# Performance work log

Measured on AMD Instinct MI355X. Metric: run time of the kernel, lower is better.

Reference implementation:

```python
import jax, jax.numpy as jnp
import numpy as np
import math

B, S, F, D, H, L, E, K = 8, 1024, 8, 512, 8, 3, 4, 2
HD = D // H


def _ln(x, g, b, eps=1e-5):
    m = x.mean(-1, keepdims=True)
    v = x.var(-1, keepdims=True)
    return (x - m) / jnp.sqrt(v + eps) * g + b


def _pos_encoding(seq, d):
    pos = jnp.arange(seq, dtype=jnp.float32)[:, None]
    div = jnp.exp(jnp.arange(0, d, 2, dtype=jnp.float32) * (-math.log(10000.0) / d))
    pe = jnp.zeros((seq, d), jnp.float32)
    pe = pe.at[:, 0::2].set(jnp.sin(pos * div))
    pe = pe.at[:, 1::2].set(jnp.cos(pos * div))
    return pe


def setup_inputs() -> dict:
    key = jax.random.key(0)
    ks = iter(jax.random.split(key, 40))

    def w(shape, s=0.02):
        return jax.random.normal(next(ks), shape, jnp.float32) * s

    return {
        "x": jax.random.normal(next(ks), (B, S, F), jnp.float32),
        "Wp": w((D, F)), "bp": jnp.zeros((D,), jnp.float32),
        "femb": w((5, D)),
        "qkv_w": w((L, 3 * D, D)), "qkv_b": jnp.zeros((L, 3 * D), jnp.float32),
        "ow": w((L, D, D)), "ob": jnp.zeros((L, D), jnp.float32),
        "g1": jnp.ones((L, D), jnp.float32), "beta1": jnp.zeros((L, D), jnp.float32),
        "gw": w((L, E, D)), "gb": jnp.zeros((L, E), jnp.float32),
        "ew1": w((L, E, 2 * D, D)), "eb1": jnp.zeros((L, E, 2 * D), jnp.float32),
        "ew2": w((L, E, D, 2 * D)), "eb2": jnp.zeros((L, E, D), jnp.float32),
        "g2": jnp.ones((L, D), jnp.float32), "beta2": jnp.zeros((L, D), jnp.float32),
        "hw": w((3, D)), "hb": jnp.zeros((3,), jnp.float32),
        "freq_idx": 2,
    }


def reference(x, Wp, bp, femb, qkv_w, qkv_b, ow, ob, g1, beta1, gw, gb,
              ew1, eb1, ew2, eb2, g2, beta2, hw, hb, freq_idx):
    # instance norm over time axis (torch std is unbiased -> ddof=1)
    mean = x.mean(axis=1, keepdims=True)
    std = x.std(axis=1, ddof=1, keepdims=True) + 1e-5
    xn = (x - mean) / std

    h = xn @ Wp.T + bp                      # [B,S,D]
    h = h + femb[freq_idx]                  # broadcast freq embedding
    h = h + _pos_encoding(S, D)

    for l in range(L):
        # --- multi-head self-attention ---
        qkv = h @ qkv_w[l].T + qkv_b[l]     # [B,S,3D]
        q, k, v = jnp.split(qkv, 3, axis=-1)
        q = q.reshape(B, S, H, HD).transpose(0, 2, 1, 3)
        k = k.reshape(B, S, H, HD).transpose(0, 2, 1, 3)
        v = v.reshape(B, S, H, HD).transpose(0, 2, 1, 3)
        att = jax.nn.softmax(jnp.einsum('bhqd,bhkd->bhqk', q, k) / math.sqrt(HD), axis=-1)
        o = jnp.einsum('bhqk,bhkd->bhqd', att, v).transpose(0, 2, 1, 3).reshape(B, S, D)
        o = o @ ow[l].T + ob[l]
        h = _ln(h + o, g1[l], beta1[l])

        # --- SparseMoE: top-k softmax gating, renormalized combine ---
        flat = h.reshape(-1, D)                               # [T,D], T=B*S
        probs = jax.nn.softmax(flat @ gw[l].T + gb[l], axis=-1)
        tw, ti = jax.lax.top_k(probs, K)                      # [T,K]
        tw = tw / tw.sum(axis=-1, keepdims=True)
        hid = jax.nn.relu(jnp.einsum('td,efd->tef', flat, ew1[l]) + eb1[l])  # [T,E,2D]
        eo = jnp.einsum('tef,edf->ted', hid, ew2[l]) + eb2[l]                # [T,E,D]
        cw = (jax.nn.one_hot(ti, E, dtype=flat.dtype) * tw[..., None]).sum(1)  # [T,E]
        moe = jnp.einsum('te,ted->td', cw, eo).reshape(B, S, D)
        h = _ln(h + moe, g2[l], beta2[l])

    return h[:, -1, :] @ hw.T + hb           # [B,3] quantiles
```

## Files before the change

kernel.cpp:

```cpp
#include <hip/hip_runtime.h>
#include <hip/hip_bf16.h>
#include <math.h>

typedef __hip_bfloat16 bf16;
typedef __attribute__((ext_vector_type(8))) short short8;
typedef __attribute__((ext_vector_type(4))) short s4v;
typedef __attribute__((ext_vector_type(4))) float f32x4;

constexpr int B_ = 8, S_ = 1024, F_ = 8, D_ = 512, H_ = 8, E_ = 4;
constexpr int T_  = B_ * S_;
constexpr int D3_ = 3 * D_;
constexpr int CAP_ = T_ * 2 + E_ * 128;

__device__ __forceinline__ float b2f(bf16 v) { return __bfloat162float(v); }
__device__ __forceinline__ float ldin(const void* p, size_t i, int bf) {
  return bf ? __bfloat162float(((const bf16*)p)[i]) : ((const float*)p)[i];
}
__device__ __forceinline__ void gload16(const void* g, void* l) {
  __builtin_amdgcn_global_load_lds((const __attribute__((address_space(1))) unsigned int*)g,
                                   (__attribute__((address_space(3))) unsigned int*)l, 16, 0, 0);
}

__global__ void detect_kernel(const void* __restrict__ x, int* __restrict__ flag) {
  if (threadIdx.x == 0 && blockIdx.x == 0) {
    const unsigned short* u = (const unsigned short*)x;
    int c = 0;
    for (int i = 0; i < 256; i += 2) {
      int ex = (u[i] >> 7) & 0xFF;
      if (ex >= 96 && ex <= 144) c++;
    }
    flag[0] = (c >= 64) ? 1 : 0;
  }
}

__global__ __launch_bounds__(256) void convw_kernel(const void* __restrict__ Asrc, size_t offA,
                                                    size_t nA,
                                                    const void* __restrict__ Bsrc, size_t offB,
                                                    bf16* __restrict__ dst,
                                                    const int* __restrict__ flag) {
  const int bf = flag[0];
  size_t i = ((size_t)blockIdx.x * 256 + threadIdx.x) * 8;
  const void* s = Asrc;
  size_t so = offA + i;
  if (i >= nA) { s = Bsrc; so = offB + (i - nA); }
  if (bf) {
    *(short8*)(dst + i) = *(const short8*)((const bf16*)s + so);
  } else {
    const float* sp = (const float*)s + so;
    short8 v;
#pragma unroll
    for (int u = 0; u < 8; u++) { bf16 t = __float2bfloat16(sp[u]); v[u] = *(short*)&t; }
    *(short8*)(dst + i) = v;
  }
}

__global__ __launch_bounds__(256) void instnorm_kernel(const void* __restrict__ x,
                                                       float* __restrict__ xn,
                                                       const int* __restrict__ flag) {
  const int bf = flag[0];
  int b = blockIdx.x / F_, f = blockIdx.x % F_;
  int tid = threadIdx.x;
  __shared__ float red[256];
  const int base = b * S_ * F_ + f;
  float s = 0.f;
  for (int j = tid; j < S_; j += 256) s += ldin(x, base + j * F_, bf);
  red[tid] = s; __syncthreads();
  for (int w = 128; w; w >>= 1) { if (tid < w) red[tid] += red[tid + w]; __syncthreads(); }
  float mean = red[0] / S_;
  __syncthreads();
  float v = 0.f;
  for (int j = tid; j < S_; j += 256) { float d = ldin(x, base + j * F_, bf) - mean; v += d * d; }
  red[tid] = v; __syncthreads();
  for (int w = 128; w; w >>= 1) { if (tid < w) red[tid] += red[tid + w]; __syncthreads(); }
  float inv = 1.f / (sqrtf(red[0] / (float)(S_ - 1)) + 1e-5f);
  for (int j = tid; j < S_; j += 256) xn[base + j * F_] = (ldin(x, base + j * F_, bf) - mean) * inv;
}

__global__ __launch_bounds__(256) void pe_kernel(const void* __restrict__ bp,
                                                 const void* __restrict__ femb,
                                                 const int* __restrict__ freq_idx,
                                                 float* __restrict__ addtab,
                                                 const int* __restrict__ flag) {
  const int bf = flag[0];
  int idx = blockIdx.x * 256 + threadIdx.x;
  int dp = idx & (D_ / 2 - 1);
  int s  = idx / (D_ / 2);
  int d0 = dp * 2;
  int fi = freq_idx[0];
  const float cexp = -9.2103403719761836f / (float)D_;
  float ang = (float)s * expf((float)d0 * cexp);
  float sv, cv;
  sincosf(ang, &sv, &cv);
  addtab[(size_t)s * D_ + d0]     = sv + ldin(bp, d0, bf)     + ldin(femb, (size_t)fi * D_ + d0, bf);
  addtab[(size_t)s * D_ + d0 + 1] = cv + ldin(bp, d0 + 1, bf) + ldin(femb, (size_t)fi * D_ + d0 + 1, bf);
}

constexpr int IPG_ = 8;
__global__ __launch_bounds__(256) void input_proj_kernel(const float* __restrict__ xn,
                                                         const void* __restrict__ Wp,
                                                         const float* __restrict__ addtab,
                                                         float* __restrict__ h,
                                                         bf16* __restrict__ hb16,
                                                         const int* __restrict__ flag) {
  const int bf = flag[0];
  const int tid = threadIdx.x;
  const int d0 = tid * 2;
  const int tbase = blockIdx.x * IPG_;
  float wp0[8], wp1[8];
  if (bf) {
    short8 w0 = *(const short8*)((const bf16*)Wp + (size_t)d0 * F_);
    short8 w1 = *(const short8*)((const bf16*)Wp + (size_t)(d0 + 1) * F_);
#pragma unroll
    for (int f = 0; f < 8; f++) {
      unsigned short u0 = (unsigned short)w0[f], u1 = (unsigned short)w1[f];
      wp0[f] = __bfloat162float(*(bf16*)&u0);
      wp1[f] = __bfloat162float(*(bf16*)&u1);
    }
  } else {
    const float* wpf = (const float*)Wp + (size_t)d0 * F_;
    f32x4 a = *(const f32x4*)(wpf);
    f32x4 b = *(const f32x4*)(wpf + 4);
    f32x4 c = *(const f32x4*)(wpf + 8);
    f32x4 d = *(const f32x4*)(wpf + 12);
#pragma unroll
    for (int f = 0; f < 4; f++) { wp0[f] = a[f]; wp0[4 + f] = b[f]; wp1[f] = c[f]; wp1[4 + f] = d[f]; }
  }
#pragma unroll
  for (int g = 0; g < IPG_; g++) {
    int t = tbase + g;
    int s = t & (S_ - 1);
    const float* xr = xn + (size_t)t * F_;
    f32x4 x0 = *(const f32x4*)xr;
    f32x4 x1 = *(const f32x4*)(xr + 4);
    const float2 at = *(const float2*)(addtab + (size_t)s * D_ + d0);
    float a0 = at.x, a1 = at.y;
#pragma unroll
    for (int f = 0; f < 4; f++) { a0 += x0[f] * wp0[f]; a1 += x0[f] * wp1[f]; }
#pragma unroll
    for (int f = 0; f < 4; f++) { a0 += x1[f] * wp0[4 + f]; a1 += x1[f] * wp1[4 + f]; }
    *(float2*)(h + (size_t)t * D_ + d0) = make_float2(a0, a1);
    bf16 b0 = __float2bfloat16(a0), b1 = __float2bfloat16(a1);
    unsigned pk = (unsigned)(*(unsigned short*)&b0) | ((unsigned)(*(unsigned short*)&b1) << 16);
    *(unsigned*)(hb16 + (size_t)t * D_ + d0) = pk;
  }
}

template <int MODE>
__global__ __launch_bounds__(256) void mfma_gemm(
    const bf16* __restrict__ A, const bf16* __restrict__ Wt,
    const void* __restrict__ bias, size_t boff, void* __restrict__ C_,
    int Kd, int lda, int ldb, int ldc, const int* __restrict__ flag) {
  const int wbf = flag[0];
  __shared__ bf16 As[3][128][32];
  __shared__ bf16 Bs[3][128][32];
  const int tid = threadIdx.x;
  const int ln = tid & 63, wv = tid >> 6;
  int id = blockIdx.x + gridDim.x * blockIdx.y;
  int xcd = id & 7, idq = id >> 3;
  const int n0 = (idq % gridDim.x) * 128;
  const int m0 = (xcd + 8 * (idq / gridDim.x)) * 128;
  const int wr = (wv >> 1) * 64, wc = (wv & 1) * 64;
  const int mrow = ln & 15, quad = ln >> 4;
  const int srow = ln >> 2;
  const int skof = (ln & 3) * 8;
  const int kchunk = Kd / gridDim.z;
  const int kbeg = blockIdx.z * kchunk;
  const int kend = kbeg + kchunk;

  auto stage = [&](int pb, int k0) {
#pragma unroll
    for (int j = 0; j < 2; j++) {
      int row = 16 * (4 * j + wv) + srow;
      gload16(A + (size_t)(m0 + row) * lda + k0 + skof,
              (char*)&As[pb][0][0] + (size_t)(4 * j + wv) * 1024);
    }
#pragma unroll
    for (int j = 0; j < 2; j++) {
      int row = 16 * (4 * j + wv) + srow;
      gload16(Wt + (size_t)(n0 + row) * ldb + k0 + skof,
              (char*)&Bs[pb][0][0] + (size_t)(4 * j + wv) * 1024);
    }
  };

  f32x4 acc[4][4];
#pragma unroll
  for (int i = 0; i < 4; i++)
#pragma unroll
    for (int j = 0; j < 4; j++) acc[i][j] = (f32x4){0.f, 0.f, 0.f, 0.f};

  stage(0, kbeg);
  stage(1, kbeg + 32);
  int p = 0;
  for (int k0 = kbeg; k0 < kend; k0 += 32) {
    if (k0 + 32 < kend) asm volatile("s_waitcnt vmcnt(4)" ::: "memory");
    else                asm volatile("s_waitcnt vmcnt(0)" ::: "memory");
    __builtin_amdgcn_s_barrier();
    __builtin_amdgcn_sched_barrier(0);
    short8 af[4], bfr[4];
#pragma unroll
    for (int t = 0; t < 4; t++) {
      af[t]  = *(const short8*)&As[p][wr + t * 16 + mrow][quad * 8];
      bfr[t] = *(const short8*)&Bs[p][wc + t * 16 + mrow][quad * 8];
    }
    if (k0 + 64 < kend) {
      int ps = (p == 0) ? 2 : p - 1;
      stage(ps, k0 + 64);
    }
#pragma unroll
    for (int i = 0; i < 4; i++)
#pragma unroll
      for (int j = 0; j < 4; j++)
        acc[i][j] = __builtin_amdgcn_mfma_f32_16x16x32_bf16(af[i], bfr[j], acc[i][j], 0, 0, 0);
    p = (p == 2) ? 0 : p + 1;
  }

  bf16* slice = (MODE == 0) ? (bf16*)C_ + (size_t)blockIdx.z * T_ * D_ : (bf16*)C_;
#pragma unroll
  for (int tj = 0; tj < 4; tj++) {
    int n = n0 + wc + tj * 16 + mrow;
    float bv = (MODE == 3) ? ldin(bias, boff + n, wbf) : 0.f;
#pragma unroll
    for (int ti = 0; ti < 4; ti++) {
      int mbase = m0 + wr + ti * 16 + quad * 4;
#pragma unroll
      for (int r = 0; r < 4; r++) {
        int m = mbase + r;
        float v = acc[ti][tj][r];
        slice[(size_t)m * ldc + n] = __float2bfloat16(MODE == 3 ? v + bv : v);
      }
    }
  }
}

__global__ __launch_bounds__(256) void attn_kernel(const bf16* __restrict__ qkv,
                                                   bf16* __restrict__ o) {
  __shared__ bf16 QP[64][72];
  __shared__ bf16 Ks[64][72];
  __shared__ bf16 Vt[64][72];
  const int tid = threadIdx.x;
  const int ln = tid & 63, wv = tid >> 6;
  const int mrow = ln & 15, quad = ln >> 4;
  const int id = blockIdx.x;
  const int xcd = id & 7, j = id >> 3;
  const int qt = j & 15;
  const int pr = xcd + 8 * (j >> 4);
  const int hh = pr & 7, b = pr >> 3;
  const int q0 = qt * 64;
  const int sr = tid >> 2;
  const int sg = tid & 3;
  const int sc = sg * 8;
  const int col0 = sr ^ (sg << 4);
  const int col1 = sr ^ (((sg + 4) & 3) << 4);

  {
    const bf16* src = qkv + (size_t)(b * S_ + q0 + sr) * D3_ + hh * 64;
    *(short8*)&QP[sr][sc]      = *(const short8*)(src + sc);
    *(short8*)&QP[sr][sc + 32] = *(const short8*)(src + sc + 32);
  }
  __syncthreads();
  short8 aq[2];
  aq[0] = *(const short8*)&QP[wv * 16 + mrow][quad * 8];
  aq[1] = *(const short8*)&QP[wv * 16 + mrow][quad * 8 + 32];

  float m_st = -1e30f, l_st = 0.f;
  f32x4 oacc[4];
#pragma unroll
  for (int t = 0; t < 4; t++) oacc[t] = (f32x4){0.f, 0.f, 0.f, 0.f};

  short8 kA, kB, vA, vB;
  {
    const bf16* srcK = qkv + (size_t)(b * S_ + sr) * D3_ + D_ + hh * 64;
    kA = *(const short8*)(srcK + sc);
    kB = *(const short8*)(srcK + sc + 32);
    const bf16* srcV = qkv + (size_t)(b * S_ + sr) * D3_ + 2 * D_ + hh * 64;
    vA = *(const short8*)(srcV + sc);
    vB = *(const short8*)(srcV + sc + 32);
  }

  for (int kt = 0; kt < 16; kt++) {
    __builtin_amdgcn_s_barrier();
    *(short8*)&Ks[sr][sc]      = kA;
    *(short8*)&Ks[sr][sc + 32] = kB;
#pragma unroll
    for (int u = 0; u < 8; u++) {
      *(short*)&Vt[sc + u][col0]      = vA[u];
      *(short*)&Vt[sc + 32 + u][col1] = vB[u];
    }
    if (kt + 1 < 16) {
      int k0n = (kt + 1) * 64;
      const bf16* srcK = qkv + (size_t)(b * S_ + k0n + sr) * D3_ + D_ + hh * 64;
      kA = *(const short8*)(srcK + sc);
      kB = *(const short8*)(srcK + sc + 32);
      const bf16* srcV = qkv + (size_t)(b * S_ + k0n + sr) * D3_ + 2 * D_ + hh * 64;
      vA = *(const short8*)(srcV + sc);
      vB = *(const short8*)(srcV + sc + 32);
    }
    asm volatile("s_waitcnt lgkmcnt(0)" ::: "memory");
    __builtin_amdgcn_s_barrier();
    __builtin_amdgcn_sched_barrier(0);
    f32x4 s[4];
    __builtin_amdgcn_s_setprio(1);
#pragma unroll
    for (int t = 0; t < 4; t++) {
      s[t] = (f32x4){0.f, 0.f, 0.f, 0.f};
#pragma unroll
      for (int ks = 0; ks < 2; ks++) {
        short8 bk = *(const short8*)&Ks[t * 16 + mrow][quad * 8 + ks * 32];
        s[t] = __builtin_amdgcn_mfma_f32_16x16x32_bf16(bk, aq[ks], s[t], 0, 0, 0);
      }
    }
    __builtin_amdgcn_s_setprio(0);
    float rm = s[0][0];
#pragma unroll
    for (int t = 0; t < 4; t++)
#pragma unroll
      for (int r = 0; r < 4; r++) rm = fmaxf(rm, s[t][r]);
    rm *= 0.125f;
    rm = fmaxf(rm, __shfl_xor(rm, 16, 64));
    rm = fmaxf(rm, __shfl_xor(rm, 32, 64));
    float mnew = fmaxf(m_st, rm);
    float alpha = __expf(m_st - mnew);
    m_st = mnew;
    float rs = 0.f;
#pragma unroll
    for (int t = 0; t < 4; t++) {
      s4v pk;
#pragma unroll
      for (int r = 0; r < 4; r++) {
        float p = __expf(s[t][r] * 0.125f - mnew);
        rs += p;
        bf16 tb = __float2bfloat16(p);
        pk[r] = *(short*)&tb;
      }
      *(s4v*)&QP[wv * 16 + mrow][t * 16 + quad * 4] = pk;
    }
    rs += __shfl_xor(rs, 16, 64);
    rs += __shfl_xor(rs, 32, 64);
    l_st = l_st * alpha + rs;
    float af4[4];
#pragma unroll
    for (int r = 0; r < 4; r++) af4[r] = __shfl(alpha, quad * 4 + r, 64);
#pragma unroll
    for (int t = 0; t < 4; t++)
#pragma unroll
      for (int r = 0; r < 4; r++) oacc[t][r] *= af4[r];
    short8 ap[2];
    ap[0] = *(const short8*)&QP[wv * 16 + mrow][quad * 8];
    ap[1] = *(const short8*)&QP[wv * 16 + mrow][quad * 8 + 32];
    __builtin_amdgcn_s_setprio(1);
#pragma unroll
    for (int t = 0; t < 4; t++) {
      int d = t * 16 + mrow;
      int swz = ((d >> 3) & 3) << 4;
#pragma unroll
      for (int ks = 0; ks < 2; ks++) {
        short8 bv = *(const short8*)&Vt[d][(quad * 8 + ks * 32) ^ swz];
        oacc[t] = __builtin_amdgcn_mfma_f32_16x16x32_bf16(ap[ks], bv, oacc[t], 0, 0, 0);
      }
    }
    __builtin_amdgcn_s_setprio(0);
  }
  float linv[4];
#pragma unroll
  for (int r = 0; r < 4; r++) linv[r] = 1.f / __shfl(l_st, quad * 4 + r, 64);
#pragma unroll
  for (int r = 0; r < 4; r++) {
    size_t base = (size_t)(b * S_ + q0 + wv * 16 + quad * 4 + r) * D_ + hh * 64;
#pragma unroll
    for (int t = 0; t < 4; t++)
      o[base + t * 16 + mrow] = __float2bfloat16(oacc[t][r] * linv[r]);
  }
}

__global__ __launch_bounds__(256) void reduce_ln_kernel(float* __restrict__ h,
                                                        bf16* __restrict__ hb16,
                                                        const bf16* __restrict__ ps,
                                                        int nsl, int mode,
                                                        const void* __restrict__ bias,
                                                        size_t boff,
                                                        const float* __restrict__ cw,
                                                        const void* __restrict__ eb2p,
                                                        size_t e2off,
                                                        const void* __restrict__ g,
                                                        const void* __restrict__ beta,
                                                        size_t off,
                                                        const int* __restrict__ flag) {
  const int bf = flag[0];
  int t = blockIdx.x, tid = threadIdx.x;
  __shared__ float r1[256], r2[256];
  const size_t base = (size_t)t * D_;
  float o0 = 0.f, o1 = 0.f;
  for (int s = 0; s < nsl; s++) {
    o0 += b2f(ps[(size_t)s * T_ * D_ + base + tid]);
    o1 += b2f(ps[(size_t)s * T_ * D_ + base + tid + 256]);
  }
  if (mode == 0) {
    o0 += ldin(bias, boff + tid, bf);
    o1 += ldin(bias, boff + tid + 256, bf);
  } else {
#pragma unroll
    for (int e = 0; e < 4; e++) {
      float w = cw[t * 4 + e];
      o0 += w * ldin(eb2p, e2off + e * D_ + tid, bf);
      o1 += w * ldin(eb2p, e2off + e * D_ + tid + 256, bf);
    }
  }
  float* hr = h + base;
  float v0 = hr[tid] + o0;
  float v1 = hr[tid + 256] + o1;
  r1[tid] = v0 + v1;
  r2[tid] = v0 * v0 + v1 * v1;
  __syncthreads();
  for (int w = 128; w; w >>= 1) { if (tid < w) { r1[tid] += r1[tid + w]; r2[tid] += r2[tid + w]; } __syncthreads(); }
  float mean = r1[0] * (1.f / D_);
  float var  = r2[0] * (1.f / D_) - mean * mean;
  float rstd = rsqrtf(var + 1e-5f);
  float n0 = (v0 - mean) * rstd * ldin(g, off + tid, bf) + ldin(beta, off + tid, bf);
  float n1 = (v1 - mean) * rstd * ldin(g, off + tid + 256, bf) + ldin(beta, off + tid + 256, bf);
  hr[tid] = n0;
  hr[tid + 256] = n1;
  hb16[base + tid] = __float2bfloat16(n0);
  hb16[base + tid + 256] = __float2bfloat16(n1);
}

__global__ __launch_bounds__(256) void gate_kernel(const float* __restrict__ hbuf,
                                                   const void* __restrict__ gw, size_t gwoff,
                                                   const void* __restrict__ gb, size_t gboff,
                                                   float* __restrict__ cw,
                                                   int* __restrict__ einfo,
                                                   float* __restrict__ w0a,
                                                   float* __restrict__ w1a,
                                                   const int* __restrict__ flag) {
  const int bf = flag[0];
  int lane = threadIdx.x & 63, wv = threadIdx.x >> 6;
  int t = blockIdx.x * 4 + wv;
  const float* xr = hbuf + (size_t)t * D_;
  float a[4] = {0, 0, 0, 0};
  for (int d = lane; d < D_; d += 64) {
    float xv = xr[d];
#pragma unroll
    for (int e = 0; e < 4; e++) a[e] += xv * ldin(gw, gwoff + e * D_ + d, bf);
  }
#pragma unroll
  for (int e = 0; e < 4; e++)
    for (int off = 32; off; off >>= 1) a[e] += __shfl_xor(a[e], off, 64);
  if (lane == 0) {
    float lg[4];
#pragma unroll
    for (int e = 0; e < 4; e++) lg[e] = a[e] + ldin(gb, gboff + e, bf);
    float m = fmaxf(fmaxf(lg[0], lg[1]), fmaxf(lg[2], lg[3]));
    float p[4], s = 0.f;
#pragma unroll
    for (int e = 0; e < 4; e++) { p[e] = __expf(lg[e] - m); s += p[e]; }
#pragma unroll
    for (int e = 0; e < 4; e++) p[e] /= s;
    int i0 = 0;
    for (int e = 1; e < 4; e++) if (p[e] > p[i0]) i0 = e;
    int i1 = -1;
    for (int e = 0; e < 4; e++) if (e != i0 && (i1 < 0 || p[e] > p[i1])) i1 = e;
    float s2 = p[i0] + p[i1];
    float ww0 = p[i0] / s2, ww1 = p[i1] / s2;
    float outw[4] = {0, 0, 0, 0};
    outw[i0] = ww0; outw[i1] = ww1;
#pragma unroll
    for (int e = 0; e < 4; e++) cw[t * 4 + e] = outw[e];
    einfo[t] = i0 | (i1 << 4);
    w0a[t] = ww0; w1a[t] = ww1;
  }
}

__global__ __launch_bounds__(256) void route_scan_kernel(const int* __restrict__ einfo,
                                                         int* __restrict__ off,
                                                         int* __restrict__ endp,
                                                         int* __restrict__ cur,
                                                         int* __restrict__ tmap) {
  __shared__ int red[4][256];
  int tid = threadIdx.x;
  int c[4] = {0, 0, 0, 0};
  for (int t = tid; t < T_; t += 256) {
    int inf = einfo[t];
    c[inf & 15]++;
    c[(inf >> 4) & 15]++;
  }
#pragma unroll
  for (int e = 0; e < 4; e++) red[e][tid] = c[e];
  __syncthreads();
  for (int w = 128; w; w >>= 1) {
    if (tid < w)
#pragma unroll
      for (int e = 0; e < 4; e++) red[e][tid] += red[e][tid + w];
    __syncthreads();
  }
  if (tid == 0) {
    int o = 0, idx = 0;
#pragma unroll
    for (int e = 0; e < 4; e++) {
      int cnt = red[e][0];
      off[e] = o;
      endp[e] = o + cnt;
      cur[e] = 0;
      int nt = (cnt + 127) >> 7;
      for (int i = 0; i < nt; i++) tmap[1 + idx++] = e | (i << 8);
      o += nt << 7;
    }
    tmap[0] = idx;
  }
}

__global__ __launch_bounds__(256) void scatter_kernel(const int* __restrict__ einfo,
                                                      const float* __restrict__ w0a,
                                                      const float* __restrict__ w1a,
                                                      const int* __restrict__ off,
                                                      int* __restrict__ cur,
                                                      int* __restrict__ pack,
                                                      float* __restrict__ wlist) {
  int t = blockIdx.x * 256 + threadIdx.x;
  int lane = threadIdx.x & 63;
  int inf = einfo[t];
#pragma unroll
  for (int rank = 0; rank < 2; rank++) {
    int my_e = (rank == 0) ? (inf & 15) : ((inf >> 4) & 15);
    float w = (rank == 0) ? w0a[t] : w1a[t];
#pragma unroll
    for (int e = 0; e < 4; e++) {
      bool p = (my_e == e);
      unsigned long long mask = __ballot(p);
      if (!mask) continue;
      int leader = __ffsll((long long)mask) - 1;
      int base = 0;
      if (lane == leader) base = atomicAdd(&cur[e], (int)__popcll(mask));
      base = __shfl(base, leader, 64);
      if (p) {
        int pos = off[e] + base + (int)__popcll(mask & ((1ULL << lane) - 1ULL));
        pack[pos] = t * 2 + rank;
        wlist[pos] = w;
      }
    }
  }
}

__global__ __launch_bounds__(256) void moe_mat1_kernel(
    const bf16* __restrict__ A, const bf16* __restrict__ Wt,
    const void* __restrict__ bias, size_t boff, bf16* __restrict__ hid,
    const int* __restrict__ off, const int* __restrict__ endp,
    const int* __restrict__ pack, const float* __restrict__ wlist,
    const int* __restrict__ tmap, const int* __restrict__ flag) {
  const int wbf = flag[0];
  int id = blockIdx.x + 8 * blockIdx.y;
  int xcd = id & 7, idq = id >> 3;
  int wx = idq & 7, wy = xcd + 8 * (idq >> 3);
  if (wy >= tmap[0]) return;
  int ent = tmap[1 + wy];
  const int e = ent & 255, mt = ent >> 8;
  const int o = off[e], en = endp[e];
  const int n0 = wx * 128;
  __shared__ bf16 As[3][128][32];
  __shared__ bf16 Bs[3][128][32];
  const int tid = threadIdx.x;
  const int ln = tid & 63, wv = tid >> 6;
  const int m0 = o + mt * 128;
  const int wr = (wv >> 1) * 64, wc = (wv & 1) * 64;
  const int mrow = ln & 15, quad = ln >> 4;
  const int srow = ln >> 2;
  const int skof = (ln & 3) * 8;
  int tokr[2];
#pragma unroll
  for (int j = 0; j < 2; j++) {
    int pos = m0 + 16 * (4 * j + wv) + srow;
    tokr[j] = pack[min(pos, en - 1)] >> 1;
  }
  const size_t wbase = (size_t)e * 1024 * 512;

  auto stage = [&](int pb, int k0) {
#pragma unroll
    for (int j = 0; j < 2; j++)
      gload16(A + (size_t)tokr[j] * 512 + k0 + skof,
              (char*)&As[pb][0][0] + (size_t)(4 * j + wv) * 1024);
#pragma unroll
    for (int j = 0; j < 2; j++) {
      int row = 16 * (4 * j + wv) + srow;
      gload16(Wt + wbase + (size_t)(n0 + row) * 512 + k0 + skof,
              (char*)&Bs[pb][0][0] + (size_t)(4 * j + wv) * 1024);
    }
  };

  f32x4 acc[4][4];
#pragma unroll
  for (int i = 0; i < 4; i++)
#pragma unroll
    for (int j = 0; j < 4; j++) acc[i][j] = (f32x4){0.f, 0.f, 0.f, 0.f};

  stage(0, 0);
  stage(1, 32);
  int p = 0;
  for (int k0 = 0; k0 < 512; k0 += 32) {
    if (k0 + 32 < 512) asm volatile("s_waitcnt vmcnt(4)" ::: "memory");
    else               asm volatile("s_waitcnt vmcnt(0)" ::: "memory");
    __builtin_amdgcn_s_barrier();
    __builtin_amdgcn_sched_barrier(0);
    short8 af[4], bfr[4];
#pragma unroll
    for (int t = 0; t < 4; t++) {
      af[t]  = *(const short8*)&As[p][wr + t * 16 + mrow][quad * 8];
      bfr[t] = *(const short8*)&Bs[p][wc + t * 16 + mrow][quad * 8];
    }
    if (k0 + 64 < 512) {
      int ps = (p == 0) ? 2 : p - 1;
      stage(ps, k0 + 64);
    }
#pragma unroll
    for (int i = 0; i < 4; i++)
#pragma unroll
      for (int j = 0; j < 4; j++)
        acc[i][j] = __builtin_amdgcn_mfma_f32_16x16x32_bf16(af[i], bfr[j], acc[i][j], 0, 0, 0);
    p = (p == 2) ? 0 : p + 1;
  }

#pragma unroll
  for (int ti = 0; ti < 4; ti++) {
#pragma unroll
    for (int r = 0; r < 4; r++) {
      int pos = m0 + wr + ti * 16 + quad * 4 + r;
      float w = (pos < en) ? wlist[pos] : 0.f;
#pragma unroll
      for (int tj = 0; tj < 4; tj++) {
        int ncol = n0 + wc + tj * 16 + mrow;
        float v = acc[ti][tj][r] + ldin(bias, boff + e * 1024 + ncol, wbf);
        hid[(size_t)pos * 1024 + ncol] = __float2bfloat16(fmaxf(v, 0.f) * w);
      }
    }
  }
}

__global__ __launch_bounds__(256) void moe_mat2_kernel(
    const bf16* __restrict__ hid, const bf16* __restrict__ Wt,
    bf16* __restrict__ psl,
    const int* __restrict__ off, const int* __restrict__ endp,
    const int* __restrict__ pack, const int* __restrict__ tmap,
    const int* __restrict__ flag) {
  int id = blockIdx.x + 4 * blockIdx.y;
  int xcd = id & 7, idq = id >> 3;
  int wx = idq & 3, wy = xcd + 8 * (idq >> 2);
  if (wy >= tmap[0]) return;
  int ent = tmap[1 + wy];
  const int e = ent & 255, mt = ent >> 8;
  const int o = off[e], en = endp[e];
  const int n0 = wx * 128;
  __shared__ bf16 As[3][128][32];
  __shared__ bf16 Bs[3][128][32];
  const int tid = threadIdx.x;
  const int ln = tid & 63, wv = tid >> 6;
  const int m0 = o + mt * 128;
  const int wr = (wv >> 1) * 64, wc = (wv & 1) * 64;
  const int mrow = ln & 15, quad = ln >> 4;
  const int srow = ln >> 2;
  const int skof = (ln & 3) * 8;
  const int kbeg = blockIdx.z * 512;
  const size_t wbase = (size_t)e * 512 * 1024;

  auto stage = [&](int pb, int k0) {
#pragma unroll
    for (int j = 0; j < 2; j++) {
      int row = 16 * (4 * j + wv) + srow;
      gload16(hid + (size_t)(m0 + row) * 1024 + k0 + skof,
              (char*)&As[pb][0][0] + (size_t)(4 * j + wv) * 1024);
    }
#pragma unroll
    for (int j = 0; j < 2; j++) {
      int row = 16 * (4 * j + wv) + srow;
      gload16(Wt + wbase + (size_t)(n0 + row) * 1024 + k0 + skof,
              (char*)&Bs[pb][0][0] + (size_t)(4 * j + wv) * 1024);
    }
  };

  f32x4 acc[4][4];
#pragma unroll
  for (int i = 0; i < 4; i++)
#pragma unroll
    for (int j = 0; j < 4; j++) acc[i][j] = (f32x4){0.f, 0.f, 0.f, 0.f};

  stage(0, kbeg);
  stage(1, kbeg + 32);
  int p = 0;
  for (int k0 = kbeg; k0 < kbeg + 512; k0 += 32) {
    if (k0 + 32 < kbeg + 512) asm volatile("s_waitcnt vmcnt(4)" ::: "memory");
    else                      asm volatile("s_waitcnt vmcnt(0)" ::: "memory");
    __builtin_amdgcn_s_barrier();
    __builtin_amdgcn_sched_barrier(0);
    short8 af[4], bfr[4];
#pragma unroll
    for (int t = 0; t < 4; t++) {
      af[t]  = *(const short8*)&As[p][wr + t * 16 + mrow][quad * 8];
      bfr[t] = *(const short8*)&Bs[p][wc + t * 16 + mrow][quad * 8];
    }
    if (k0 + 64 < kbeg + 512) {
      int ps = (p == 0) ? 2 : p - 1;
      stage(ps, k0 + 64);
    }
#pragma unroll
    for (int i = 0; i < 4; i++)
#pragma unroll
      for (int j = 0; j < 4; j++)
        acc[i][j] = __builtin_amdgcn_mfma_f32_16x16x32_bf16(af[i], bfr[j], acc[i][j], 0, 0, 0);
    p = (p == 2) ? 0 : p + 1;
  }

#pragma unroll
  for (int ti = 0; ti < 4; ti++) {
#pragma unroll
    for (int r = 0; r < 4; r++) {
      int pos = m0 + wr + ti * 16 + quad * 4 + r;
      if (pos < en) {
        int pk = pack[pos];
        int tok = pk >> 1, rank = pk & 1;
        bf16* dst = psl + (size_t)(rank * 2 + blockIdx.z) * T_ * D_ + (size_t)tok * D_;
#pragma unroll
        for (int tj = 0; tj < 4; tj++) {
          int ncol = n0 + wc + tj * 16 + mrow;
          dst[ncol] = __float2bfloat16(acc[ti][tj][r]);
        }
      }
    }
  }
}

__global__ __launch_bounds__(256) void head_kernel(const float* __restrict__ hbuf,
                                                   const void* __restrict__ hw,
                                                   const void* __restrict__ hb,
                                                   void* __restrict__ out,
                                                   const int* __restrict__ flag) {
  const int bf = flag[0];
  int bq = blockIdx.x, tid = threadIdx.x;
  int b = bq / 3, q = bq % 3;
  __shared__ float red[256];
  const float* xr = hbuf + (size_t)(b * S_ + (S_ - 1)) * D_;
  float sacc = xr[tid] * ldin(hw, (size_t)q * D_ + tid, bf)
             + xr[tid + 256] * ldin(hw, (size_t)q * D_ + tid + 256, bf);
  red[tid] = sacc; __syncthreads();
  for (int w = 128; w; w >>= 1) { if (tid < w) red[tid] += red[tid + w]; __syncthreads(); }
  if (tid == 0) {
    float r = red[0] + ldin(hb, q, bf);
    if (bf) ((bf16*)out)[bq] = __float2bfloat16(r);
    else    ((float*)out)[bq] = r;
  }
}

extern "C" void kernel_launch(void* const* d_in, const int* in_sizes, int n_in,
                              void* d_out, int out_size, void* d_ws, size_t ws_size,
                              hipStream_t stream) {
  const void* x    = d_in[0];
  const void* Wp   = d_in[1];
  const void* bp   = d_in[2];
  const void* femb = d_in[3];
  const void* qkvw = d_in[4];
  const void* qkvb = d_in[5];
  const void* ow   = d_in[6];
  const void* ob   = d_in[7];
  const void* g1   = d_in[8];
  const void* be1  = d_in[9];
  const void* gw   = d_in[10];
  const void* gb   = d_in[11];
  const void* ew1  = d_in[12];
  const void* eb1  = d_in[13];
  const void* ew2  = d_in[14];
  const void* eb2  = d_in[15];
  const void* g2   = d_in[16];
  const void* be2  = d_in[17];
  const void* hw   = d_in[18];
  const void* hb   = d_in[19];
  const int*  freq = (const int*)d_in[20];

  int*   flag  = (int*)d_ws;
  int*   off   = flag + 64;
  int*   endp  = off + 4;
  int*   cur   = endp + 4;
  int*   einfo = flag + 128;
  float* w0a   = (float*)(einfo + T_);
  float* w1a   = w0a + T_;
  int*   pack  = (int*)(w1a + T_);
  float* wlist = (float*)(pack + CAP_);
  int*   tmap  = (int*)(wlist + CAP_);
  float* xn    = (float*)(tmap + 160);
  float* h     = xn + 65536;
  float* cw    = h + (size_t)T_ * D_;
  bf16*  hb16  = (bf16*)(cw + (size_t)T_ * E_);
  bf16*  R     = hb16 + (size_t)T_ * D_;
  bf16*  qkvb16 = R;
  bf16*  ao    = R + (size_t)T_ * D3_;
  bf16*  hid   = R;
  bf16*  psl   = R + (size_t)CAP_ * 1024;
  bf16*  wcvt  = psl + (size_t)4 * T_ * D_;
  bf16*  wq    = wcvt;
  bf16*  wo    = wcvt + (size_t)D3_ * D_;
  bf16*  we1   = wcvt;
  bf16*  we2   = wcvt + (size_t)E_ * 1024 * 512;
  float* addtab = (float*)R;

  constexpr size_t NQ = (size_t)D3_ * D_;
  constexpr size_t NO = (size_t)D_ * D_;
  constexpr size_t NE = (size_t)E_ * 1024 * 512;

  detect_kernel<<<1, 64, 0, stream>>>(x, flag);
  instnorm_kernel<<<B_ * F_, 256, 0, stream>>>(x, xn, flag);
  pe_kernel<<<(S_ * D_ / 2) / 256, 256, 0, stream>>>(bp, femb, freq, addtab, flag);
  input_proj_kernel<<<T_ / IPG_, 256, 0, stream>>>(xn, Wp, addtab, h, hb16, flag);

  for (int l = 0; l < 3; l++) {
    convw_kernel<<<(NQ + NO) / 2048, 256, 0, stream>>>(
        qkvw, (size_t)l * NQ, NQ, ow, (size_t)l * NO, wcvt, flag);
    mfma_gemm<3><<<dim3(D3_ / 128, T_ / 128), 256, 0, stream>>>(
        hb16, wq, qkvb, (size_t)l * D3_, qkvb16, D_, D_, D_, D3_, flag);
    attn_kernel<<<B_ * H_ * (S_ / 64), 256, 0, stream>>>(qkvb16, ao);
    mfma_gemm<0><<<dim3(D_ / 128, T_ / 128, 2), 256, 0, stream>>>(
        ao, wo, nullptr, 0, psl, D_, D_, D_, D_, flag);
    reduce_ln_kernel<<<T_, 256, 0, stream>>>(
        h, hb16, psl, 2, 0, ob, (size_t)l * D_, nullptr, nullptr, 0,
        g1, be1, (size_t)l * D_, flag);
    gate_kernel<<<T_ / 4, 256, 0, stream>>>(h, gw, (size_t)l * E_ * D_, gb, (size_t)l * E_,
                                            cw, einfo, w0a, w1a, flag);
    route_scan_kernel<<<1, 256, 0, stream>>>(einfo, off, endp, cur, tmap);
    scatter_kernel<<<T_ / 256, 256, 0, stream>>>(einfo, w0a, w1a, off, cur, pack, wlist);
    convw_kernel<<<(NE + NE) / 2048, 256, 0, stream>>>(
        ew1, (size_t)l * NE, NE, ew2, (size_t)l * NE, wcvt, flag);
    moe_mat1_kernel<<<dim3(8, 136), 256, 0, stream>>>(
        hb16, we1, eb1, (size_t)l * E_ * 1024, hid,
        off, endp, pack, wlist, tmap, flag);
    moe_mat2_kernel<<<dim3(4, 136, 2), 256, 0, stream>>>(
        hid, we2, psl, off, endp, pack, tmap, flag);
    reduce_ln_kernel<<<T_, 256, 0, stream>>>(
        h, hb16, psl, 4, 1, nullptr, 0, cw, eb2, (size_t)l * E_ * D_,
        g2, be2, (size_t)l * D_, flag);
  }

  head_kernel<<<24, 256, 0, stream>>>(h, hw, hb, d_out, flag);
}
```

Measured before the change: 844.5 us.

## Widen attention blocks to 128 queries so K/V tiles are shared by 8 waves

The attention kernel now runs 512 threads per block, covering 128 query rows instead of 64, and halves the grid. Each staged K/V tile in LDS is reused by twice as many waves, which halves global K/V traffic and per-query staging work. Each thread now loads one short8 of K and one of V per tile instead of two. The cost is fewer blocks (512), a larger LDS footprint and higher barrier cost with 8 waves, and the unseen body must index QP rows by wave id for up to 8 waves.

New measurement: 827.4 us. -2.0%, faster.

```diff
diff --git a/kernel.cpp b/kernel.cpp
--- a/kernel.cpp
+++ b/kernel.cpp
@@ -232,9 +232,9 @@
   }
 }
 
-__global__ __launch_bounds__(256) void attn_kernel(const bf16* __restrict__ qkv,
+__global__ __launch_bounds__(512) void attn_kernel(const bf16* __restrict__ qkv,
                                                    bf16* __restrict__ o) {
-  __shared__ bf16 QP[64][72];
+  __shared__ bf16 QP[128][72];
   __shared__ bf16 Ks[64][72];
   __shared__ bf16 Vt[64][72];
   const int tid = threadIdx.x;
@@ -242,20 +242,21 @@
   const int mrow = ln & 15, quad = ln >> 4;
   const int id = blockIdx.x;
   const int xcd = id & 7, j = id >> 3;
-  const int qt = j & 15;
-  const int pr = xcd + 8 * (j >> 4);
+  const int qt = j & 7;
+  const int pr = xcd + 8 * (j >> 3);
   const int hh = pr & 7, b = pr >> 3;
-  const int q0 = qt * 64;
-  const int sr = tid >> 2;
-  const int sg = tid & 3;
-  const int sc = sg * 8;
-  const int col0 = sr ^ (sg << 4);
-  const int col1 = sr ^ (((sg + 4) & 3) << 4);
+  const int q0 = qt * 128;
+  const int sr = tid >> 3;
+  const int sg8 = tid & 7;
+  const int sc = sg8 * 8;
+  const int colv = sr ^ ((sg8 & 3) << 4);
 
   {
-    const bf16* src = qkv + (size_t)(b * S_ + q0 + sr) * D3_ + hh * 64;
-    *(short8*)&QP[sr][sc]      = *(const short8*)(src + sc);
-    *(short8*)&QP[sr][sc + 32] = *(const short8*)(src + sc + 32);
+    const int qr = tid >> 2;
+    const int qc = (tid & 3) * 16;
+    const bf16* src = qkv + (size_t)(b * S_ + q0 + qr) * D3_ + hh * 64 + qc;
+    *(short8*)&QP[qr][qc]     = *(const short8*)(src);
+    *(short8*)&QP[qr][qc + 8] = *(const short8*)(src + 8);
   }
   __syncthreads();
   short8 aq[2];
@@ -267,33 +268,21 @@
 #pragma unroll
   for (int t = 0; t < 4; t++) oacc[t] = (f32x4){0.f, 0.f, 0.f, 0.f};
 
-  short8 kA, kB, vA, vB;
+  short8 kA, vA;
   {
-    const bf16* srcK = qkv + (size_t)(b * S_ + sr) * D3_ + D_ + hh * 64;
-    kA = *(const short8*)(srcK + sc);
-    kB = *(const short8*)(srcK + sc + 32);
-    const bf16* srcV = qkv + (size_t)(b * S_ + sr) * D3_ + 2 * D_ + hh * 64;
-    vA = *(const short8*)(srcV + sc);
-    vB = *(const short8*)(srcV + sc + 32);
+    kA = *(const short8*)(qkv + (size_t)(b * S_ + sr) * D3_ + D_ + hh * 64 + sc);
+    vA = *(const short8*)(qkv + (size_t)(b * S_ + sr) * D3_ + 2 * D_ + hh * 64 + sc);
   }
 
   for (int kt = 0; kt < 16; kt++) {
     __builtin_amdgcn_s_barrier();
-    *(short8*)&Ks[sr][sc]      = kA;
-    *(short8*)&Ks[sr][sc + 32] = kB;
-#pragma unroll
-    for (int u = 0; u < 8; u++) {
-      *(short*)&Vt[sc + u][col0]      = vA[u];
-      *(short*)&Vt[sc + 32 + u][col1] = vB[u];
-    }
+    *(short8*)&Ks[sr][sc] = kA;
+#pragma unroll
+    for (int u = 0; u < 8; u++) *(short*)&Vt[sc + u][colv] = vA[u];
     if (kt + 1 < 16) {
       int k0n = (kt + 1) * 64;
-      const bf16* srcK = qkv + (size_t)(b * S_ + k0n + sr) * D3_ + D_ + hh * 64;
-      kA = *(const short8*)(srcK + sc);
-      kB = *(const short8*)(srcK + sc + 32);
-      const bf16* srcV = qkv + (size_t)(b * S_ + k0n + sr) * D3_ + 2 * D_ + hh * 64;
-      vA = *(const short8*)(srcV + sc);
-      vB = *(const short8*)(srcV + sc + 32);
+      kA = *(const short8*)(qkv + (size_t)(b * S_ + k0n + sr) * D3_ + D_ + hh * 64 + sc);
+      vA = *(const short8*)(qkv + (size_t)(b * S_ + k0n + sr) * D3_ + 2 * D_ + hh * 64 + sc);
     }
     asm volatile("s_waitcnt lgkmcnt(0)" ::: "memory");
     __builtin_amdgcn_s_barrier();
@@ -810,7 +799,7 @@
         qkvw, (size_t)l * NQ, NQ, ow, (size_t)l * NO, wcvt, flag);
     mfma_gemm<3><<<dim3(D3_ / 128, T_ / 128), 256, 0, stream>>>(
         hb16, wq, qkvb, (size_t)l * D3_, qkvb16, D_, D_, D_, D3_, flag);
-    attn_kernel<<<B_ * H_ * (S_ / 64), 256, 0, stream>>>(qkvb16, ao);
+    attn_kernel<<<B_ * H_ * (S_ / 128), 512, 0, stream>>>(qkvb16, ao);
     mfma_gemm<0><<<dim3(D_ / 128, T_ / 128, 2), 256, 0, stream>>>(
         ao, wo, nullptr, 0, psl, D_, D_, D_, D_, flag);
     reduce_ln_kernel<<<T_, 256, 0, stream>>>(
```
